# Kernel optimization log

Hardware: AMD Instinct MI355X
Metric: run time of the kernel (lower is better)

## Reference

```python
import math
import jax, jax.numpy as jnp
import numpy as np
from jax import lax

W_DIM = 512
UP = 2
K = 3
LRELU_GAIN = math.sqrt(2.0)  # bias_act def_gain for 'lrelu'
CLAMP = 256.0                # conv_clamp * gain(=1)


def setup_inputs() -> dict:
    key = jax.random.key(0)
    ks = jax.random.split(key, 8)
    B, Cin, Cout, H = 16, 512, 512, 32
    return {
        "x": jax.random.normal(ks[0], (B, Cin, H, H), jnp.float32),
        "w_latent": jax.random.normal(ks[1], (B, W_DIM), jnp.float32),
        "affine_weight": jax.random.normal(ks[2], (Cin, W_DIM), jnp.float32),
        "affine_bias": jnp.ones((Cin,), jnp.float32),  # bias_init=1
        "conv_weight": jax.random.normal(ks[3], (Cout, Cin, K, K), jnp.float32),
        "noise": jax.random.normal(ks[4], (B, 1, 2 * H, 2 * H), jnp.float32),
        "noise_strength": jax.random.uniform(ks[5], (1,), jnp.float32),
        "bias": jax.random.normal(ks[6], (Cout,), jnp.float32),
    }


def reference(x, w_latent, affine_weight, affine_bias, conv_weight, noise, noise_strength, bias):
    B, Cin, H, W = x.shape
    Cout = conv_weight.shape[0]

    # EqualFullyConnectedLayer (linear act): style = w @ (W * 1/sqrt(in)).T + b
    style = w_latent @ (affine_weight * (1.0 / math.sqrt(W_DIM))).T + affine_bias  # [B, Cin]

    # Modulate + demodulate per-sample weights: [B, Cout, Cin, K, K]
    wmod = conv_weight[None] * style[:, None, :, None, None]
    dcoefs = lax.rsqrt(jnp.sum(wmod * wmod, axis=(2, 3, 4)) + 1e-8)  # [B, Cout]
    wmod = wmod * dcoefs[:, :, None, None, None]

    # Grouped transposed conv (stride=UP), batch-as-groups trick.
    # torch.conv_transpose2d(x, w.transpose, stride=UP) == dilated conv with
    # spatially-flipped modulated weight, lhs_dilation=UP, padding=K-1.
    w_eff = wmod.reshape(B * Cout, Cin, K, K)[:, :, ::-1, ::-1]
    x1 = x.reshape(1, B * Cin, H, W)
    y = lax.conv_general_dilated(
        x1, w_eff, window_strides=(1, 1),
        padding=[(K - 1, K - 1), (K - 1, K - 1)],
        lhs_dilation=(UP, UP), feature_group_count=B,
        dimension_numbers=("NCHW", "OIHW", "NCHW"))  # [1, B*Cout, 2H+1, 2W+1]

    # upfirdn2d: FIR low-pass (1,3,3,1) outer, normalized, gain=up^2, pad (1,1,1,1)
    f1 = jnp.array([1.0, 3.0, 3.0, 1.0], jnp.float32)
    f2 = jnp.outer(f1, f1)
    f2 = f2 / f2.sum() * (UP * UP)
    yc = y.reshape(B * Cout, 1, 2 * H + 1, 2 * W + 1)
    y = lax.conv_general_dilated(
        yc, f2[None, None], window_strides=(1, 1), padding=[(1, 1), (1, 1)],
        dimension_numbers=("NCHW", "OIHW", "NCHW"))
    y = y.reshape(B, Cout, 2 * H, 2 * W)

    # noise injection + fused bias + lrelu(gain=sqrt(2)) + clamp
    y = y + noise * noise_strength[0]
    y = y + bias[None, :, None, None]
    y = jax.nn.leaky_relu(y, negative_slope=0.2) * LRELU_GAIN
    return jnp.clip(y, -CLAMP, CLAMP)
```

## Files before the change

kernel.cpp:

```cpp
#include <hip/hip_runtime.h>
#include <hip/hip_bf16.h>


typedef unsigned short u16;
typedef unsigned int u32;
typedef u16 u16x8 __attribute__((ext_vector_type(8)));
typedef __bf16 bf16x8 __attribute__((ext_vector_type(8)));
typedef float f32x4 __attribute__((ext_vector_type(4)));

#define NB 16

__device__ __forceinline__ float bf2f(u16 v) {
  unsigned int u = ((unsigned int)v) << 16;
  float f;
  __builtin_memcpy(&f, &u, 4);
  return f;
}
__device__ __forceinline__ u16 f2bf(float f) {
  __hip_bfloat16 h = __float2bfloat16(f);
  u16 r;
  __builtin_memcpy(&r, &h, 2);
  return r;
}
__device__ __forceinline__ void async16(u16* lds, const u16* g) {
  __builtin_amdgcn_global_load_lds(
      (const __attribute__((address_space(1))) u32*)g,
      (__attribute__((address_space(3))) u32*)lds, 16, 0, 0);
}

__global__ __launch_bounds__(256) void k_style(const float* __restrict__ wl,
                                               const float* __restrict__ aw,
                                               const float* __restrict__ ab,
                                               float* __restrict__ style) {
  __shared__ float lw[512];
  const int b = blockIdx.y;
  const int c0 = blockIdx.x << 6;
  const int t = threadIdx.x;
  for (int k = t; k < 512; k += 256) lw[k] = wl[b * 512 + k];
  __syncthreads();
  const int w = t >> 6, l = t & 63;
  const float4 lv0 = *(const float4*)(lw + (l << 2));
  const float4 lv1 = *(const float4*)(lw + 256 + (l << 2));
  for (int r = w; r < 64; r += 4) {
    const int c = c0 + r;
    const float* row = aw + (size_t)c * 512 + (l << 2);
    const float4 a0 = *(const float4*)(row);
    const float4 a1 = *(const float4*)(row + 256);
    float acc = lv0.x * a0.x + lv0.y * a0.y + lv0.z * a0.z + lv0.w * a0.w +
                lv1.x * a1.x + lv1.y * a1.y + lv1.z * a1.z + lv1.w * a1.w;
#pragma unroll
    for (int off = 32; off; off >>= 1) acc += __shfl_down(acc, off, 64);
    if (l == 0) style[b * 512 + c] = acc * 0.04419417382415922f + ab[c];
  }
}

__global__ __launch_bounds__(256) void k_wprep(const float* __restrict__ cw,
                                               const float* __restrict__ style,
                                               float* __restrict__ dcoef,
                                               u16* __restrict__ W2) {
  __shared__ u16 lw[4608];
  __shared__ float wsq[512];
  const int o = blockIdx.x, t = threadIdx.x;
  const float* src = cw + (size_t)o * 4608;
  for (int v = t; v < 4608; v += 256) {
    unsigned c = (unsigned)v / 9u;
    unsigned kp = (unsigned)v % 9u;
    lw[kp * 512 + c] = f2bf(src[v]);
  }
  for (int c = t; c < 512; c += 256) {
    const float* p = src + (size_t)c * 9;
    float s = 0.f;
#pragma unroll
    for (int k = 0; k < 9; ++k) {
      float v = p[k];
      s += v * v;
    }
    wsq[c] = s;
  }
  __syncthreads();
  u16* dst = W2 + (size_t)o * 4608;
  for (int v = t; v < 576; v += 256)
    *(u16x8*)(dst + v * 8) = *(const u16x8*)(lw + v * 8);
  const int w = t >> 6, l = t & 63;
  for (int b = w; b < NB; b += 4) {
    float part = 0.f;
#pragma unroll
    for (int c = l; c < 512; c += 64) {
      float st = style[b * 512 + c];
      part += st * st * wsq[c];
    }
#pragma unroll
    for (int off = 32; off; off >>= 1) part += __shfl_down(part, off, 64);
    if (l == 0) dcoef[b * 512 + o] = 1.0f / sqrtf(part + 1e-8f);
  }
}

__global__ __launch_bounds__(256) void k_xt(const float* __restrict__ x,
                                            const float* __restrict__ style,
                                            u16* __restrict__ xT) {
  __shared__ u16 tile[64 * 66];
  const int b = blockIdx.z, c0 = blockIdx.y << 6, s0 = blockIdx.x << 6;
  const int t = threadIdx.x;
#pragma unroll
  for (int i = 0; i < 16; ++i) {
    int e = i * 256 + t;
    int cc = e >> 6, ss = e & 63;
    int c = c0 + cc;
    float v = x[(size_t)(b * 512 + c) * 1024 + s0 + ss] * style[b * 512 + c];
    tile[cc * 66 + ss] = f2bf(v);
  }
  __syncthreads();
#pragma unroll
  for (int e = 0; e < 2; ++e) {
    int idx = e * 256 + t;
    int sc = idx >> 3;
    int cg = (idx & 7) << 3;
    u16x8 v;
#pragma unroll
    for (int g = 0; g < 8; ++g) v[g] = tile[(cg + g) * 66 + sc];
    *(u16x8*)(xT + (size_t)(b * 1024 + s0 + sc) * 512 + c0 + cg) = v;
  }
}

__global__ __launch_bounds__(512, 2) void k_gemm(const u16* __restrict__ W2,
                                                 const u16* __restrict__ xT,
                                                 u16* __restrict__ Z) {
  __shared__ union SM {
    struct { u16 A[4][8192]; u16 B[4][8192]; } g;
    u16 C[256 * 264];
  } sm;
  const int t = threadIdx.x;
  const int m0 = blockIdx.y << 8;
  const int n0 = blockIdx.x << 8;
  const int l = t & 63;
  const int w = t >> 6;
  const int wm = w >> 2;
  const int wn = w & 3;
  const int lrow = l & 15;
  const int lk = l >> 4;

  const int sr = t >> 2;
  const int sch = ((t & 3) + (sr >> 1)) & 3;
  const u16* gA = W2 + (size_t)(m0 + sr) * 512 + (sch << 3);
  const u16* gB = xT + (size_t)(n0 + sr) * 512 + (sch << 3);
  const int wb = w << 9;

  const int sk8 = ((lk - (lrow >> 1)) & 3) << 3;
  const int arow = (wm << 7) + lrow;
  const int brow = (wn << 6) + lrow;

  f32x4 acc[8][4] = {};

#define STAGE_A(nb_, kt_)                                   \
  async16(&sm.g.A[nb_][wb], gA + (kt_) * 32);               \
  async16(&sm.g.A[nb_][4096 + wb], gA + (kt_) * 32 + 65536)
#define STAGE_B(nb_, kt_)                                   \
  async16(&sm.g.B[nb_][wb], gB + (kt_) * 32);               \
  async16(&sm.g.B[nb_][4096 + wb], gB + (kt_) * 32 + 65536)

  STAGE_A(0, 0);
  STAGE_B(0, 0);
  STAGE_A(1, 1);
  STAGE_B(1, 1);
  STAGE_A(2, 2);
  STAGE_B(2, 2);
  asm volatile("s_waitcnt vmcnt(8)" ::: "memory");
  asm volatile("s_barrier" ::: "memory");

  for (int kt = 0; kt < 16; ++kt) {
    const int buf = kt & 3;
    const int nb = (kt + 3) & 3;
    const u16* Ab = sm.g.A[buf];
    const u16* Bb = sm.g.B[buf];
    bf16x8 av[4], av2[4], bv[4];
#pragma unroll
    for (int i = 0; i < 4; ++i)
      av[i] = *(const bf16x8*)(Ab + (arow + i * 16) * 32 + sk8);
#pragma unroll
    for (int i = 0; i < 4; ++i)
      av2[i] = *(const bf16x8*)(Ab + (arow + 64 + i * 16) * 32 + sk8);
#pragma unroll
    for (int j = 0; j < 4; ++j)
      bv[j] = *(const bf16x8*)(Bb + (brow + j * 16) * 32 + sk8);
    if (kt < 13) {
      STAGE_A(nb, kt + 3);
      STAGE_B(nb, kt + 3);
    }
    asm volatile("s_waitcnt lgkmcnt(0)" ::: "memory");
    __builtin_amdgcn_sched_barrier(0);
    __builtin_amdgcn_s_setprio(1);
#pragma unroll
    for (int i = 0; i < 4; ++i)
#pragma unroll
      for (int j = 0; j < 4; ++j)
        acc[i][j] = __builtin_amdgcn_mfma_f32_16x16x32_bf16(av[i], bv[j], acc[i][j], 0, 0, 0);
#pragma unroll
    for (int i = 0; i < 4; ++i)
#pragma unroll
      for (int j = 0; j < 4; ++j)
        acc[i + 4][j] = __builtin_amdgcn_mfma_f32_16x16x32_bf16(av2[i], bv[j], acc[i + 4][j], 0, 0, 0);
    __builtin_amdgcn_s_setprio(0);
    if (kt <= 12) {
      asm volatile("s_waitcnt vmcnt(8)" ::: "memory");
      asm volatile("s_barrier" ::: "memory");
    } else if (kt == 13) {
      asm volatile("s_waitcnt vmcnt(4)" ::: "memory");
      asm volatile("s_barrier" ::: "memory");
    } else if (kt == 14) {
      asm volatile("s_waitcnt vmcnt(0)" ::: "memory");
      asm volatile("s_barrier" ::: "memory");
    }
  }
#undef STAGE_A
#undef STAGE_B

  __syncthreads();
  const int crow0 = (wm << 7) + (lk << 2);
  const int ccol0 = (wn << 6) + lrow;
#pragma unroll
  for (int i = 0; i < 8; ++i)
#pragma unroll
    for (int j = 0; j < 4; ++j)
#pragma unroll
      for (int r = 0; r < 4; ++r)
        sm.C[(crow0 + i * 16 + r) * 264 + ccol0 + j * 16] = f2bf(acc[i][j][r]);
  __syncthreads();
  u16* zb = Z + (size_t)m0 * 16384 + n0;
#pragma unroll
  for (int k = 0; k < 16; ++k) {
    int c = (k << 9) | t;
    int row = c >> 5;
    int c8 = (c & 31) << 3;
    *(u16x8*)(zb + (size_t)row * 16384 + c8) = *(const u16x8*)(sm.C + row * 264 + c8);
  }
}

__global__ __launch_bounds__(512) void k_scatter(
    const u16* __restrict__ Z, const float* __restrict__ dcoef,
    const float* __restrict__ noise, const float* __restrict__ nstr,
    const float* __restrict__ bias, float* __restrict__ out) {
  __shared__ u16 Zl[9 * 1024];
  __shared__ float Hl[3 * 2048];
  const int o = blockIdx.x;
  const int b = blockIdx.y;
  const int t = threadIdx.x;
  const u16* Zp = Z + (size_t)o * 9 * 16384 + (size_t)b * 1024;
  for (int v = t; v < 1152; v += 512) {
    int kp = v >> 7, off = (v & 127) << 3;
    *(u16x8*)(Zl + kp * 1024 + off) = *(const u16x8*)(Zp + (size_t)kp * 16384 + off);
  }
  __syncthreads();
#pragma unroll
  for (int e = 0; e < 6; ++e) {
    int idx = e * 512 + t;
    int ky = idx >> 10;
    int i = (idx >> 5) & 31;
    int j = idx & 31;
    const u16* P0 = Zl + (ky * 3 + 0) * 1024 + i * 32;
    const u16* P1 = P0 + 1024;
    const u16* P2 = P0 + 2048;
    float Ej = bf2f(P0[j]) + (j >= 1 ? bf2f(P2[j - 1]) : 0.f);
    float Ej1 = (j < 31 ? bf2f(P0[j + 1]) : 0.f) + bf2f(P2[j]);
    float Ojm = j >= 1 ? bf2f(P1[j - 1]) : 0.f;
    float Oj = bf2f(P1[j]);
    float Ojp = j < 31 ? bf2f(P1[j + 1]) : 0.f;
    float* hp = Hl + ky * 2048 + i * 64 + j;
    hp[0] = Ojm + 3.f * Ej + 3.f * Oj + Ej1;
    hp[32] = Ej + 3.f * Oj + 3.f * Ej1 + Ojp;
  }
  __syncthreads();
  const float dc = dcoef[b * 512 + o] * 0.0625f;
  const float ns = nstr[0];
  const float bo = bias[o];
  const int n = t & 63;
  const int i0 = (t >> 6) << 2;
  const int sw = ((n & 1) << 5) | (n >> 1);
  const float* H0 = Hl + sw;
  const float* H1 = Hl + 2048 + sw;
  const float* H2 = Hl + 4096 + sw;
  float h0 = H0[i0 * 64];
  float h1 = H1[i0 * 64];
  float h1p = (i0 > 0) ? H1[(i0 - 1) * 64] : 0.f;
  float h2p = (i0 > 0) ? H2[(i0 - 1) * 64] : 0.f;
  const float* nz = noise + ((size_t)b << 12) + n;
  float* op = out + (((size_t)(b * 512 + o)) << 12) + n;
#pragma unroll
  for (int s = 0; s < 4; ++s) {
    int i = i0 + s;
    float h0n = (i < 31) ? H0[(i + 1) * 64] : 0.f;
    float h1n = (i < 31) ? H1[(i + 1) * 64] : 0.f;
    float h2 = H2[i * 64];
    float ev = h1p + 3.f * (h0 + h2p) + 3.f * h1 + (h0n + h2);
    float od = (h0 + h2p) + 3.f * h1 + 3.f * (h0n + h2) + h1n;
    int m = 2 * i;
    float v0 = ev * dc + nz[(size_t)m * 64] * ns + bo;
    v0 = (v0 > 0.f ? v0 : 0.2f * v0) * 1.4142135623730951f;
    v0 = fminf(fmaxf(v0, -256.f), 256.f);
    op[(size_t)m * 64] = v0;
    float v1 = od * dc + nz[(size_t)(m + 1) * 64] * ns + bo;
    v1 = (v1 > 0.f ? v1 : 0.2f * v1) * 1.4142135623730951f;
    v1 = fminf(fmaxf(v1, -256.f), 256.f);
    op[(size_t)(m + 1) * 64] = v1;
    h0 = h0n;
    h1p = h1;
    h1 = h1n;
    h2p = h2;
  }
}

extern "C" void kernel_launch(void* const* d_in, const int* in_sizes, int n_in,
                              void* d_out, int out_size, void* d_ws, size_t ws_size,
                              hipStream_t stream) {
  const float* x = (const float*)d_in[0];
  const float* wl = (const float*)d_in[1];
  const float* aw = (const float*)d_in[2];
  const float* ab = (const float*)d_in[3];
  const float* cw = (const float*)d_in[4];
  const float* noise = (const float*)d_in[5];
  const float* nstr = (const float*)d_in[6];
  const float* bias = (const float*)d_in[7];
  float* out = (float*)d_out;

  float* style = (float*)d_ws;
  float* dcoef = style + 8192;
  u16* W2 = (u16*)(dcoef + 8192);
  u16* xT = W2 + 4608 * 512;
  u16* Z = xT + (size_t)16384 * 512;

  k_style<<<dim3(8, 16), 256, 0, stream>>>(wl, aw, ab, style);
  k_wprep<<<dim3(512), 256, 0, stream>>>(cw, style, dcoef, W2);
  k_xt<<<dim3(16, 8, 16), 256, 0, stream>>>(x, style, xT);
  k_gemm<<<dim3(64, 18), 512, 0, stream>>>(W2, xT, Z);
  k_scatter<<<dim3(512, 16), 512, 0, stream>>>(Z, dcoef, noise, nstr, bias, out);
}
```

Measured before the change: 354.1 us.

## Restructure GEMM main loop into double-buffered 64-wide K tiles with interleaved staging

The 4-stage, 32-wide-K pipeline in the GEMM kernel is replaced by a 2-buffer scheme where each buffer holds two 32-wide K halves, so each iteration covers 64 of K. Each iteration is split into four MFMA phases, with A/B global-to-LDS loads for the next tile issued between phases and barriers around them, in the style of ping-pong scheduling. The aim is to overlap memory traffic with MFMA work at finer granularity and cut register pressure by reusing one av buffer. In exchange it adds many more s_barrier points per iteration and leaves less prefetch distance.

```diff
diff --git a/kernel.cpp b/kernel.cpp
--- a/kernel.cpp
+++ b/kernel.cpp
@@ -126,7 +126,7 @@
                                                  const u16* __restrict__ xT,
                                                  u16* __restrict__ Z) {
   __shared__ union SM {
-    struct { u16 A[4][8192]; u16 B[4][8192]; } g;
+    struct { u16 A[2][2][8192]; u16 B[2][2][8192]; } g;
     u16 C[256 * 264];
   } sm;
   const int t = threadIdx.x;
@@ -143,7 +143,7 @@
   const int sch = ((t & 3) + (sr >> 1)) & 3;
   const u16* gA = W2 + (size_t)(m0 + sr) * 512 + (sch << 3);
   const u16* gB = xT + (size_t)(n0 + sr) * 512 + (sch << 3);
-  const int wb = w << 9;
+  const int stg = t << 3;
 
   const int sk8 = ((lk - (lrow >> 1)) & 3) << 3;
   const int arow = (wm << 7) + lrow;
@@ -151,41 +151,39 @@
 
   f32x4 acc[8][4] = {};
 
-#define STAGE_A(nb_, kt_)                                   \
-  async16(&sm.g.A[nb_][wb], gA + (kt_) * 32);               \
-  async16(&sm.g.A[nb_][4096 + wb], gA + (kt_) * 32 + 65536)
-#define STAGE_B(nb_, kt_)                                   \
-  async16(&sm.g.B[nb_][wb], gB + (kt_) * 32);               \
-  async16(&sm.g.B[nb_][4096 + wb], gB + (kt_) * 32 + 65536)
-
-  STAGE_A(0, 0);
-  STAGE_B(0, 0);
-  STAGE_A(1, 1);
-  STAGE_B(1, 1);
-  STAGE_A(2, 2);
-  STAGE_B(2, 2);
-  asm volatile("s_waitcnt vmcnt(8)" ::: "memory");
+#define STG_A(buf_, kh_, kt_)                                          \
+  async16(&sm.g.A[buf_][kh_][stg], gA + (kt_) * 64 + (kh_) * 32);      \
+  async16(&sm.g.A[buf_][kh_][4096 + stg],                              \
+          gA + (kt_) * 64 + (kh_) * 32 + 128 * 512)
+#define STG_B(buf_, kh_, kt_)                                          \
+  async16(&sm.g.B[buf_][kh_][stg], gB + (kt_) * 64 + (kh_) * 32);      \
+  async16(&sm.g.B[buf_][kh_][4096 + stg],                              \
+          gB + (kt_) * 64 + (kh_) * 32 + 128 * 512)
+
+  STG_A(0, 0, 0);
+  STG_B(0, 0, 0);
+  STG_A(0, 1, 0);
+  STG_B(0, 1, 0);
+  asm volatile("s_waitcnt vmcnt(4)" ::: "memory");
   asm volatile("s_barrier" ::: "memory");
 
-  for (int kt = 0; kt < 16; ++kt) {
-    const int buf = kt & 3;
-    const int nb = (kt + 3) & 3;
-    const u16* Ab = sm.g.A[buf];
-    const u16* Bb = sm.g.B[buf];
-    bf16x8 av[4], av2[4], bv[4];
-#pragma unroll
-    for (int i = 0; i < 4; ++i)
-      av[i] = *(const bf16x8*)(Ab + (arow + i * 16) * 32 + sk8);
-#pragma unroll
-    for (int i = 0; i < 4; ++i)
-      av2[i] = *(const bf16x8*)(Ab + (arow + 64 + i * 16) * 32 + sk8);
+  for (int kt = 0; kt < 8; ++kt) {
+    const int buf = kt & 1;
+    const int nxt = buf ^ 1;
+    const u16* Ak0 = sm.g.A[buf][0];
+    const u16* Ak1 = sm.g.A[buf][1];
+    const u16* Bk0 = sm.g.B[buf][0];
+    const u16* Bk1 = sm.g.B[buf][1];
+    bf16x8 av[4], bv[4];
+
+#pragma unroll
+    for (int i = 0; i < 4; ++i)
+      av[i] = *(const bf16x8*)(Ak0 + (arow + i * 16) * 32 + sk8);
 #pragma unroll
     for (int j = 0; j < 4; ++j)
-      bv[j] = *(const bf16x8*)(Bb + (brow + j * 16) * 32 + sk8);
-    if (kt < 13) {
-      STAGE_A(nb, kt + 3);
-      STAGE_B(nb, kt + 3);
-    }
+      bv[j] = *(const bf16x8*)(Bk0 + (brow + j * 16) * 32 + sk8);
+    if (kt < 7) { STG_A(nxt, 0, kt + 1); }
+    asm volatile("s_barrier" ::: "memory");
     asm volatile("s_waitcnt lgkmcnt(0)" ::: "memory");
     __builtin_amdgcn_sched_barrier(0);
     __builtin_amdgcn_s_setprio(1);
@@ -194,25 +192,70 @@
 #pragma unroll
       for (int j = 0; j < 4; ++j)
         acc[i][j] = __builtin_amdgcn_mfma_f32_16x16x32_bf16(av[i], bv[j], acc[i][j], 0, 0, 0);
+    __builtin_amdgcn_s_setprio(0);
+    asm volatile("s_barrier" ::: "memory");
+
+#pragma unroll
+    for (int i = 0; i < 4; ++i)
+      av[i] = *(const bf16x8*)(Ak0 + (arow + 64 + i * 16) * 32 + sk8);
+    if (kt < 7) { STG_B(nxt, 0, kt + 1); }
+    asm volatile("s_barrier" ::: "memory");
+    asm volatile("s_waitcnt lgkmcnt(0)" ::: "memory");
+    __builtin_amdgcn_sched_barrier(0);
+    __builtin_amdgcn_s_setprio(1);
 #pragma unroll
     for (int i = 0; i < 4; ++i)
 #pragma unroll
       for (int j = 0; j < 4; ++j)
-        acc[i + 4][j] = __builtin_amdgcn_mfma_f32_16x16x32_bf16(av2[i], bv[j], acc[i + 4][j], 0, 0, 0);
+        acc[i + 4][j] = __builtin_amdgcn_mfma_f32_16x16x32_bf16(av[i], bv[j], acc[i + 4][j], 0, 0, 0);
     __builtin_amdgcn_s_setprio(0);
-    if (kt <= 12) {
-      asm volatile("s_waitcnt vmcnt(8)" ::: "memory");
-      asm volatile("s_barrier" ::: "memory");
-    } else if (kt == 13) {
+    if (kt < 7) {
       asm volatile("s_waitcnt vmcnt(4)" ::: "memory");
-      asm volatile("s_barrier" ::: "memory");
-    } else if (kt == 14) {
+    } else {
       asm volatile("s_waitcnt vmcnt(0)" ::: "memory");
-      asm volatile("s_barrier" ::: "memory");
     }
-  }
-#undef STAGE_A
-#undef STAGE_B
+    asm volatile("s_barrier" ::: "memory");
+
+#pragma unroll
+    for (int i = 0; i < 4; ++i)
+      av[i] = *(const bf16x8*)(Ak1 + (arow + i * 16) * 32 + sk8);
+#pragma unroll
+    for (int j = 0; j < 4; ++j)
+      bv[j] = *(const bf16x8*)(Bk1 + (brow + j * 16) * 32 + sk8);
+    if (kt < 7) { STG_A(nxt, 1, kt + 1); }
+    asm volatile("s_barrier" ::: "memory");
+    asm volatile("s_waitcnt lgkmcnt(0)" ::: "memory");
+    __builtin_amdgcn_sched_barrier(0);
+    __builtin_amdgcn_s_setprio(1);
+#pragma unroll
+    for (int i = 0; i < 4; ++i)
+#pragma unroll
+      for (int j = 0; j < 4; ++j)
+        acc[i][j] = __builtin_amdgcn_mfma_f32_16x16x32_bf16(av[i], bv[j], acc[i][j], 0, 0, 0);
+    __builtin_amdgcn_s_setprio(0);
+    asm volatile("s_barrier" ::: "memory");
+
+#pragma unroll
+    for (int i = 0; i < 4; ++i)
+      av[i] = *(const bf16x8*)(Ak1 + (arow + 64 + i * 16) * 32 + sk8);
+    if (kt < 7) { STG_B(nxt, 1, kt + 1); }
+    asm volatile("s_barrier" ::: "memory");
+    asm volatile("s_waitcnt lgkmcnt(0)" ::: "memory");
+    __builtin_amdgcn_sched_barrier(0);
+    __builtin_amdgcn_s_setprio(1);
+#pragma unroll
+    for (int i = 0; i < 4; ++i)
+#pragma unroll
+      for (int j = 0; j < 4; ++j)
+        acc[i + 4][j] = __builtin_amdgcn_mfma_f32_16x16x32_bf16(av[i], bv[j], acc[i + 4][j], 0, 0, 0);
+    __builtin_amdgcn_s_setprio(0);
+    if (kt < 7) {
+      asm volatile("s_waitcnt vmcnt(4)" ::: "memory");
+    }
+    asm volatile("s_barrier" ::: "memory");
+  }
+#undef STG_A
+#undef STG_B
 
   __syncthreads();
   const int crow0 = (wm << 7) + (lk << 2);
```

Measured after the change: 349.4 us. No clear change (-1.3%).

## Shrink GEMM M-tile to 128 with 3-stage pipeline for higher occupancy

Applied to the files above, without the earlier changes.

Halves the GEMM block tile along M from 256 to 128 rows and doubles the grid in that dimension. The LDS ring buffer drops from four stages to three, and each thread now holds a 4x4 accumulator instead of 8x4. This shrinks LDS and register use so that four 512-thread blocks per CU are requested instead of two, aiming at better latency hiding and tail balance. The cost is lower arithmetic intensity per block, meaning more redundant B-tile loads from global memory and a shallower prefetch depth.

```diff
diff --git a/kernel.cpp b/kernel.cpp
--- a/kernel.cpp
+++ b/kernel.cpp
@@ -122,15 +122,15 @@
   }
 }
 
-__global__ __launch_bounds__(512, 2) void k_gemm(const u16* __restrict__ W2,
+__global__ __launch_bounds__(512, 4) void k_gemm(const u16* __restrict__ W2,
                                                  const u16* __restrict__ xT,
                                                  u16* __restrict__ Z) {
   __shared__ union SM {
-    struct { u16 A[4][8192]; u16 B[4][8192]; } g;
-    u16 C[256 * 264];
+    struct { u16 A[3][4096]; u16 B[3][8192]; } g;
+    u16 C[128 * 264];
   } sm;
   const int t = threadIdx.x;
-  const int m0 = blockIdx.y << 8;
+  const int m0 = blockIdx.y << 7;
   const int n0 = blockIdx.x << 8;
   const int l = t & 63;
   const int w = t >> 6;
@@ -143,49 +143,36 @@
   const int sch = ((t & 3) + (sr >> 1)) & 3;
   const u16* gA = W2 + (size_t)(m0 + sr) * 512 + (sch << 3);
   const u16* gB = xT + (size_t)(n0 + sr) * 512 + (sch << 3);
-  const int wb = w << 9;
+  const int stg = t << 3;
 
   const int sk8 = ((lk - (lrow >> 1)) & 3) << 3;
-  const int arow = (wm << 7) + lrow;
+  const int arow = (wm << 6) + lrow;
   const int brow = (wn << 6) + lrow;
 
-  f32x4 acc[8][4] = {};
-
-#define STAGE_A(nb_, kt_)                                   \
-  async16(&sm.g.A[nb_][wb], gA + (kt_) * 32);               \
-  async16(&sm.g.A[nb_][4096 + wb], gA + (kt_) * 32 + 65536)
-#define STAGE_B(nb_, kt_)                                   \
-  async16(&sm.g.B[nb_][wb], gB + (kt_) * 32);               \
-  async16(&sm.g.B[nb_][4096 + wb], gB + (kt_) * 32 + 65536)
-
-  STAGE_A(0, 0);
-  STAGE_B(0, 0);
-  STAGE_A(1, 1);
-  STAGE_B(1, 1);
-  STAGE_A(2, 2);
-  STAGE_B(2, 2);
-  asm volatile("s_waitcnt vmcnt(8)" ::: "memory");
+  f32x4 acc[4][4] = {};
+
+#define STG(buf_, kt_)                                              \
+  async16(&sm.g.A[buf_][stg], gA + (kt_) * 32);                     \
+  async16(&sm.g.B[buf_][stg], gB + (kt_) * 32);                     \
+  async16(&sm.g.B[buf_][4096 + stg], gB + (kt_) * 32 + 128 * 512)
+
+  STG(0, 0);
+  STG(1, 1);
+  asm volatile("s_waitcnt vmcnt(3)" ::: "memory");
   asm volatile("s_barrier" ::: "memory");
 
+  int buf = 0, nxt = 2;
   for (int kt = 0; kt < 16; ++kt) {
-    const int buf = kt & 3;
-    const int nb = (kt + 3) & 3;
     const u16* Ab = sm.g.A[buf];
     const u16* Bb = sm.g.B[buf];
-    bf16x8 av[4], av2[4], bv[4];
+    bf16x8 av[4], bv[4];
 #pragma unroll
     for (int i = 0; i < 4; ++i)
       av[i] = *(const bf16x8*)(Ab + (arow + i * 16) * 32 + sk8);
 #pragma unroll
-    for (int i = 0; i < 4; ++i)
-      av2[i] = *(const bf16x8*)(Ab + (arow + 64 + i * 16) * 32 + sk8);
-#pragma unroll
     for (int j = 0; j < 4; ++j)
       bv[j] = *(const bf16x8*)(Bb + (brow + j * 16) * 32 + sk8);
-    if (kt < 13) {
-      STAGE_A(nb, kt + 3);
-      STAGE_B(nb, kt + 3);
-    }
+    if (kt < 14) { STG(nxt, kt + 2); }
     asm volatile("s_waitcnt lgkmcnt(0)" ::: "memory");
     __builtin_amdgcn_sched_barrier(0);
     __builtin_amdgcn_s_setprio(1);
@@ -194,31 +181,23 @@
 #pragma unroll
       for (int j = 0; j < 4; ++j)
         acc[i][j] = __builtin_amdgcn_mfma_f32_16x16x32_bf16(av[i], bv[j], acc[i][j], 0, 0, 0);
-#pragma unroll
-    for (int i = 0; i < 4; ++i)
-#pragma unroll
-      for (int j = 0; j < 4; ++j)
-        acc[i + 4][j] = __builtin_amdgcn_mfma_f32_16x16x32_bf16(av2[i], bv[j], acc[i + 4][j], 0, 0, 0);
     __builtin_amdgcn_s_setprio(0);
-    if (kt <= 12) {
-      asm volatile("s_waitcnt vmcnt(8)" ::: "memory");
-      asm volatile("s_barrier" ::: "memory");
-    } else if (kt == 13) {
-      asm volatile("s_waitcnt vmcnt(4)" ::: "memory");
-      asm volatile("s_barrier" ::: "memory");
+    if (kt <= 13) {
+      asm volatile("s_waitcnt vmcnt(3)" ::: "memory");
     } else if (kt == 14) {
       asm volatile("s_waitcnt vmcnt(0)" ::: "memory");
-      asm volatile("s_barrier" ::: "memory");
     }
-  }
-#undef STAGE_A
-#undef STAGE_B
-
-  __syncthreads();
-  const int crow0 = (wm << 7) + (lk << 2);
+    asm volatile("s_barrier" ::: "memory");
+    buf = (buf == 2) ? 0 : buf + 1;
+    nxt = (nxt == 2) ? 0 : nxt + 1;
+  }
+#undef STG
+
+  __syncthreads();
+  const int crow0 = (wm << 6) + (lk << 2);
   const int ccol0 = (wn << 6) + lrow;
 #pragma unroll
-  for (int i = 0; i < 8; ++i)
+  for (int i = 0; i < 4; ++i)
 #pragma unroll
     for (int j = 0; j < 4; ++j)
 #pragma unroll
@@ -227,7 +206,7 @@
   __syncthreads();
   u16* zb = Z + (size_t)m0 * 16384 + n0;
 #pragma unroll
-  for (int k = 0; k < 16; ++k) {
+  for (int k = 0; k < 8; ++k) {
     int c = (k << 9) | t;
     int row = c >> 5;
     int c8 = (c & 31) << 3;
@@ -330,6 +309,6 @@
   k_style<<<dim3(8, 16), 256, 0, stream>>>(wl, aw, ab, style);
   k_wprep<<<dim3(512), 256, 0, stream>>>(cw, style, dcoef, W2);
   k_xt<<<dim3(16, 8, 16), 256, 0, stream>>>(x, style, xT);
-  k_gemm<<<dim3(64, 18), 512, 0, stream>>>(W2, xT, Z);
+  k_gemm<<<dim3(64, 36), 512, 0, stream>>>(W2, xT, Z);
   k_scatter<<<dim3(512, 16), 512, 0, stream>>>(Z, dcoef, noise, nstr, bias, out);
 }
```

Result: faster. 338.3 us (-4.5%).
